# Kernel tuning notes

Hardware: AMD Instinct MI355X
Metric: run time of the kernel (lower is better)

The kernel has to match this reference:

```python
import jax, jax.numpy as jnp
import numpy as np

B, S, H, KV, D = 1, 2048, 16, 4, 128
HID = H * D
CACHE = 2048
EPS = 1e-6
SCALE = 128 ** -0.5  # query_pre_attn_scalar ** -0.5
NEG = -1e9


def setup_inputs() -> dict:
    key = jax.random.key(0)
    ks = jax.random.split(key, 12)
    hidden_states = jax.random.normal(ks[0], (B, S, HID), jnp.float32)
    # rotary embeddings (Gemma3 style, base 10000, half-dim frequencies)
    pos = jnp.arange(S, dtype=jnp.float32)[:, None]
    inv_freq = 1.0 / (10000.0 ** (jnp.arange(0, D, 2, dtype=jnp.float32) / D))
    freqs = pos * inv_freq[None, :]
    emb = jnp.concatenate([freqs, freqs], axis=-1)  # [S, D]
    cos = jnp.cos(emb)[None]  # [1, S, D]
    sin = jnp.sin(emb)[None]
    # additive causal mask [B, 1, S, S]
    r = jnp.arange(S)
    attention_mask = jnp.where(r[:, None] >= r[None, :], 0.0, NEG).astype(jnp.float32)[None, None]
    lyra_key_cache = jax.random.normal(ks[1], (1, KV, CACHE, D), jnp.float32)
    lyra_value_cache = jax.random.normal(ks[2], (1, KV, CACHE, D), jnp.float32)
    w = 0.02
    Wq = jax.random.normal(ks[3], (H * D, HID), jnp.float32) * w
    Wk = jax.random.normal(ks[4], (KV * D, HID), jnp.float32) * w
    Wv = jax.random.normal(ks[5], (KV * D, HID), jnp.float32) * w
    Wo = jax.random.normal(ks[6], (HID, H * D), jnp.float32) * w
    q_norm_w = jax.random.normal(ks[7], (D,), jnp.float32) * 0.1
    k_norm_w = jax.random.normal(ks[8], (D,), jnp.float32) * 0.1
    return dict(hidden_states=hidden_states, cos=cos, sin=sin,
                attention_mask=attention_mask,
                lyra_key_cache=lyra_key_cache, lyra_value_cache=lyra_value_cache,
                Wq=Wq, Wk=Wk, Wv=Wv, Wo=Wo, q_norm_w=q_norm_w, k_norm_w=k_norm_w)


def _rmsnorm(x, w):
    xf = x.astype(jnp.float32)
    n = xf * jax.lax.rsqrt(jnp.mean(xf * xf, axis=-1, keepdims=True) + EPS)
    return (n * (1.0 + w.astype(jnp.float32))).astype(x.dtype)


def _rotate_half(x):
    h = x.shape[-1] // 2
    return jnp.concatenate([-x[..., h:], x[..., :h]], axis=-1)


def _rope(x, c, s):
    return x * c + _rotate_half(x) * s


def _attend(q, k, v, mask, n_rep):
    # q: [B,h,Sq,D]; k,v: [B,KV,Sk,D]; mask additive float broadcastable to [B,h,Sq,Sk]
    k = jnp.repeat(k, n_rep, axis=1)
    v = jnp.repeat(v, n_rep, axis=1)
    w = jnp.einsum('bhqd,bhkd->bhqk', q, k) * SCALE + mask
    w = jax.nn.softmax(w.astype(jnp.float32), axis=-1).astype(q.dtype)
    out = jnp.einsum('bhqk,bhkd->bhqd', w, v)
    return out, w


def reference(hidden_states, cos, sin, attention_mask, lyra_key_cache,
              lyra_value_cache, Wq, Wk, Wv, Wo, q_norm_w, k_norm_w):
    bsz, q_len, _ = hidden_states.shape
    q = (hidden_states @ Wq.T).reshape(bsz, q_len, H, D).transpose(0, 2, 1, 3)
    k = (hidden_states @ Wk.T).reshape(bsz, q_len, KV, D).transpose(0, 2, 1, 3)
    v = (hidden_states @ Wv.T).reshape(bsz, q_len, KV, D).transpose(0, 2, 1, 3)
    q = _rmsnorm(q, q_norm_w)
    k = _rmsnorm(k, k_norm_w)
    vanilla_q, lyra_q = q[:, :H // 2], q[:, H // 2:]
    c = cos[:, None]  # [B,1,S,D]
    s = sin[:, None]
    n_rep = (H // 2) // KV  # stream_num_key_value_groups
    # vanilla stream
    vanilla_q_rope = _rope(vanilla_q, c, s)
    k_rope = _rope(k, c, s)
    vanilla_out, vanilla_w = _attend(vanilla_q_rope, k_rope, v, attention_mask, n_rep)
    # lyra stream: prepend static KV cache; bool mask added as float (faithful to source)
    lyra_q_rope = _rope(lyra_q, c, s)
    lk = jnp.concatenate([jnp.broadcast_to(lyra_key_cache, (bsz, KV, CACHE, D)), k_rope], axis=2)
    lv = jnp.concatenate([jnp.broadcast_to(lyra_value_cache, (bsz, KV, CACHE, D)), v], axis=2)
    rows = jnp.arange(q_len)[:, None]
    cols = jnp.arange(CACHE + q_len)[None, :]
    lyra_mask = (rows < cols - CACHE).astype(jnp.float32)[None, None]  # True -> +1.0, as in torch code
    lyra_out, _ = _attend(lyra_q_rope, lk, lv, lyra_mask, n_rep)
    combined = jnp.concatenate([vanilla_out, lyra_out], axis=1)  # [B,H,S,D]
    combined = combined.transpose(0, 2, 1, 3).reshape(bsz, q_len, H * D)
    attn_output = combined @ Wo.T
    return attn_output, vanilla_w
```

## Files before the change

kernel.cpp:

```cpp
#include <hip/hip_runtime.h>
#include <math.h>

#define S_LEN 2048
#define HID 2048
#define NH 16
#define NKV 4
#define DH 128
#define CACHE_LEN 2048
#define QKV_W 3072
#define SCALE 0.08838834764831845f
#define EPS 1e-6f
#define LYRA_C 12.0f

typedef short bf16x8 __attribute__((ext_vector_type(8)));
typedef float f32x4 __attribute__((ext_vector_type(4)));

static __device__ __forceinline__ short f2bf(float x) {
  union { float f; unsigned u; } v; v.f = x;
  unsigned r = (v.u + 0x7FFF + ((v.u >> 16) & 1)) >> 16;
  return (short)r;
}

static __device__ __forceinline__ float bf2f(short h) {
  union { unsigned u; float f; } v;
// ... 123 lines not shown
  const int rem = e4 & ((1 << 19) - 1);
  const int key = rem >> 7;
  const int d = rem & 127;
  const int dsw = d ^ ((key & 7) << 3);
  if (key < CACHE_LEN) {
    float4 v = *(const float4*)(kcache + (((size_t)kvh * CACHE_LEN + key) << 7) + d);
    short4 o;
    o.x = f2bf(v.x); o.y = f2bf(v.y); o.z = f2bf(v.z); o.w = f2bf(v.w);
    *(short4*)(Kbf + (size_t)(e4 - d) + dsw) = o;
  } else {
    float4 v = *(const float4*)(qkv + (size_t)(key - CACHE_LEN) * QKV_W + 2048 + kvh * DH + d);
    short4 o;
    o.x = f2bf(v.x); o.y = f2bf(v.y); o.z = f2bf(v.z); o.w = f2bf(v.w);
    *(short4*)(Kbf + (size_t)(e4 - d) + dsw) = o;
    short4 ol;
    ol.x = f2bf(v.x - bf2f(o.x));
    ol.y = f2bf(v.y - bf2f(o.y));
    ol.z = f2bf(v.z - bf2f(o.z));
    ol.w = f2bf(v.w - bf2f(o.w));
    *(short4*)(Klo + ((size_t)kvh * 2048 + (key - CACHE_LEN)) * 128 + dsw) = ol;
  }
}

__global__ __launch_bounds__(256) void pack_vt(
    const float* __restrict__ qkv, const float* __restrict__ vcache,
    short* __restrict__ Vt) {
  __shared__ float tile[64][65];
  const int key0 = blockIdx.x * 64;
  const int d0 = blockIdx.y * 64;
  const int kvh = blockIdx.z;
  const int t = threadIdx.x;
  const int c = t & 63;
  const int r0 = t >> 6;
#pragma unroll
  for (int i = 0; i < 16; ++i) {
    int r = r0 + i * 4;
    int key = key0 + r;
    float v;
    if (key < CACHE_LEN)
      v = vcache[(((size_t)kvh * CACHE_LEN + key) << 7) + d0 + c];
    else
      v = qkv[(size_t)(key - CACHE_LEN) * QKV_W + 2560 + kvh * DH + d0 + c];
    tile[r][c] = v;
  }
  __syncthreads();
#pragma unroll
  for (int i = 0; i < 16; ++i) {
    int wr = r0 + i * 4;
    int csw = c ^ (((d0 + wr) & 7) << 3);
    Vt[((size_t)kvh * DH + d0 + wr) * 4096 + key0 + csw] = f2bf(tile[c][wr]);
  }
}

static __device__ __forceinline__ void stage_kv(
    const short* Kb, const short* Vb, short* buf, int key0, int w, int lane) {
#pragma unroll
  for (int i = 0; i < 2; ++i)
    GLDS16(Kb + ((size_t)key0 + w * 8 + i * 4) * 128 + lane * 8,
           buf + (w * 8 + i * 4) * 128);
#pragma unroll
  for (int j = 0; j < 2; ++j)
    GLDS16(Vb + (size_t)(w * 16 + j * 8 + (lane >> 3)) * 4096 + key0 +
               (lane & 7) * 8,
           buf + 8192 + (w * 16 + j * 8) * 64);
}

__global__ __launch_bounds__(512) void lyra_attn(
    const float* __restrict__ qkv,
    const short* __restrict__ Kbf,
    const short* __restrict__ Vtb,
    short* __restrict__ combined_bf) {
  __shared__ short sKV[3][16384];
  __shared__ short sP[8][16][64];
  __shared__ float sL[64];
  const int hj = blockIdx.x;
  const int qt = blockIdx.y;
  const int kvh = hj >> 1;
  const int t = threadIdx.x;
  const int w = t >> 6;
  const int lane = t & 63;
  const int quad = lane >> 4;
  const int l16 = lane & 15;
  const int wr = w >> 1;
  const int wc = w & 1;
  const int row0 = qt * 64;
  const int rbase = row0 + wr * 16 + quad * 4;
  const int swx = (l16 & 7) << 4;

  bf16x8 qf[4];
  {
    const float* qrow =
        qkv + (size_t)(row0 + wr * 16 + l16) * QKV_W + (8 + hj) * DH;
#pragma unroll
    for (int ks = 0; ks < 4; ++ks) {
      float4 f0 = *(const float4*)(qrow + ks * 32 + quad * 8);
      float4 f1 = *(const float4*)(qrow + ks * 32 + quad * 8 + 4);
      qf[ks][0] = f2bf(f0.x); qf[ks][1] = f2bf(f0.y);
      qf[ks][2] = f2bf(f0.z); qf[ks][3] = f2bf(f0.w);
      qf[ks][4] = f2bf(f1.x); qf[ks][5] = f2bf(f1.y);
      qf[ks][6] = f2bf(f1.z); qf[ks][7] = f2bf(f1.w);
    }
  }
  bf16x8 onesf;
#pragma unroll
  for (int i = 0; i < 8; ++i) onesf[i] = (short)0x3F80;

  f32x4 accO[8];
#pragma unroll
  for (int i = 0; i < 8; ++i) accO[i] = (f32x4){0.f, 0.f, 0.f, 0.f};
  f32x4 accL = (f32x4){0.f, 0.f, 0.f, 0.f};

  const short* Kb = Kbf + (size_t)kvh * 4096 * DH;
  const short* Vb = Vtb + (size_t)kvh * DH * 4096;

  stage_kv(Kb, Vb, &sKV[0][0], 0, w, lane);
  stage_kv(Kb, Vb, &sKV[1][0], 64, w, lane);

  short* sPw = &sP[w][0][0];
  int b = 0;
  for (int kt = 0; kt < 64; ++kt) {
    asm volatile("s_waitcnt vmcnt(4)" ::: "memory");
    __builtin_amdgcn_s_barrier();
    __builtin_amdgcn_sched_barrier(0);

    {
      int nb = b + 2; if (nb >= 3) nb -= 3;
      stage_kv(Kb, Vb, &sKV[nb][0], ((kt + 2) & 63) * 64, w, lane);
    }

    const char* Ksc = (const char*)&sKV[b][0];
    const char* Vsc = (const char*)&sKV[b][8192];

    f32x4 accS[2];
#pragma unroll
    for (int s = 0; s < 2; ++s) accS[s] = (f32x4){0.f, 0.f, 0.f, 0.f};
    __builtin_amdgcn_s_setprio(1);
#pragma unroll
    for (int s = 0; s < 2; ++s) {
      const char* krow = Ksc + (wc * 32 + s * 16 + l16) * 256;
#pragma unroll
      for (int ks = 0; ks < 4; ++ks) {
        bf16x8 bk = *(const bf16x8*)(krow + ((ks * 64 + quad * 16) ^ swx));
        accS[s] = __builtin_amdgcn_mfma_f32_16x16x32_bf16(qf[ks], bk, accS[s],
                                                          0, 0, 0);
      }
    }
    __builtin_amdgcn_s_setprio(0);

    const int base = kt * 64 + wc * 32;
    if (kt >= 32) {
#pragma unroll
      for (int s = 0; s < 2; ++s) {
        const int col = base + s * 16 + l16;
#pragma unroll
        for (int r = 0; r < 4; ++r) {
          const int row = quad * 4 + r;
          float sc = accS[s][r] * SCALE;
          if ((col - CACHE_LEN) > (rbase + r)) sc += 1.0f;
          const int sl = (s * 2 + (l16 >> 3)) ^ (row & 7);
          sPw[row * 64 + sl * 8 + (l16 & 7)] = f2bf(__expf(sc - LYRA_C));
        }
      }
    } else {
#pragma unroll
      for (int s = 0; s < 2; ++s)
#pragma unroll
        for (int r = 0; r < 4; ++r) {
          const int row = quad * 4 + r;
          const int sl = (s * 2 + (l16 >> 3)) ^ (row & 7);
          sPw[row * 64 + sl * 8 + (l16 & 7)] =
              f2bf(__expf(accS[s][r] * SCALE - LYRA_C));
        }
    }

    __builtin_amdgcn_s_setprio(1);
    bf16x8 ap = *(const bf16x8*)&sPw[l16 * 64 + ((quad ^ (l16 & 7)) << 3)];
    accL = __builtin_amdgcn_mfma_f32_16x16x32_bf16(ap, onesf, accL, 0, 0, 0);
#pragma unroll
    for (int t8 = 0; t8 < 8; ++t8) {
      bf16x8 bv = *(const bf16x8*)(
          Vsc + (t8 * 16 + l16) * 128 + ((wc * 64 + quad * 16) ^ swx));
      accO[t8] = __builtin_amdgcn_mfma_f32_16x16x32_bf16(ap, bv, accO[t8],
                                                         0, 0, 0);
    }
    __builtin_amdgcn_s_setprio(0);

    ++b; if (b == 3) b = 0;
  }

  __syncthreads();
  float* sO = (float*)&sKV[0][0];
  if (wc == 1) {
#pragma unroll
    for (int t8 = 0; t8 < 8; ++t8)
#pragma unroll
      for (int r = 0; r < 4; ++r)
        sO[((wr * 16 + quad * 4 + r) << 7) + t8 * 16 + l16] = accO[t8][r];
    if (l16 == 0) {
#pragma unroll
      for (int r = 0; r < 4; ++r) sL[wr * 16 + quad * 4 + r] = accL[r];
    }
  }
  __syncthreads();
  if (wc == 0) {
    float linv[4];
#pragma unroll
    for (int r = 0; r < 4; ++r)
      linv[r] = 1.0f / (accL[r] + sL[wr * 16 + quad * 4 + r]);
#pragma unroll
    for (int t8 = 0; t8 < 8; ++t8)
#pragma unroll
      for (int r = 0; r < 4; ++r) {
        float o = accO[t8][r] + sO[((wr * 16 + quad * 4 + r) << 7) + t8 * 16 + l16];
        combined_bf[(size_t)(rbase + r) * HID + (8 + hj) * DH + t8 * 16 + l16] =
            f2bf(o * linv[r]);
      }
  }
}

static __device__ __forceinline__ void stage_van(
    const short* Kh, const short* Kl, const short* Vb, short* buf,
    int key0, int w, int lane) {
#pragma unroll
  for (int i = 0; i < 2; ++i) {
    GLDS16(Kh + ((size_t)key0 + w * 8 + i * 4) * 128 + lane * 8,
           buf + (w * 8 + i * 4) * 128);
    GLDS16(Kl + ((size_t)key0 + w * 8 + i * 4) * 128 + lane * 8,
           buf + 8192 + (w * 8 + i * 4) * 128);
  }
#pragma unroll
  for (int j = 0; j < 2; ++j)
    GLDS16(Vb + (size_t)(w * 16 + j * 8 + (lane >> 3)) * 4096 + key0 +
               (lane & 7) * 8,
           buf + 16384 + (w * 16 + j * 8) * 64);
}

__global__ __launch_bounds__(512) void vanilla_attn(
    const float* __restrict__ qkv,
    const short* __restrict__ Kbf,
    const short* __restrict__ Klo,
    const short* __restrict__ Vtb,
    float* __restrict__ wout,
    float* __restrict__ vinv,
    short* __restrict__ combined_bf) {
  __shared__ short sKV[2][24576];
  __shared__ short sP[8][16][64];
  __shared__ float sL[64];
  const int hj = blockIdx.x;
  const int qt = blockIdx.y;
  const int kvh = hj >> 1;
  const int t = threadIdx.x;
  const int w = t >> 6;
  const int lane = t & 63;
  const int quad = lane >> 4;
  const int l16 = lane & 15;
  const int wr = w >> 1;
  const int wc = w & 1;
  const int row0 = qt * 64;
  const int rbase = row0 + wr * 16 + quad * 4;
  const int swx = (l16 & 7) << 4;

  bf16x8 qh[4], ql[4];
  {
    const float* qrow =
        qkv + (size_t)(row0 + wr * 16 + l16) * QKV_W + hj * DH;
#pragma unroll
    for (int ks = 0; ks < 4; ++ks) {
#pragma unroll
      for (int e = 0; e < 8; ++e) {
        float x = qrow[ks * 32 + quad * 8 + e];
        short h = f2bf(x);
        qh[ks][e] = h;
        ql[ks][e] = f2bf(x - bf2f(h));
      }
    }
  }

  f32x4 accO[8];
#pragma unroll
  for (int i = 0; i < 8; ++i) accO[i] = (f32x4){0.f, 0.f, 0.f, 0.f};
  float accR[4] = {0.f, 0.f, 0.f, 0.f};

  const short* Kh = Kbf + ((size_t)kvh * 4096 + 2048) * DH;
  const short* Kl = Klo + (size_t)kvh * 2048 * DH;
  const short* Vb = Vtb + (size_t)kvh * DH * 4096 + 2048;
  float* wrow = wout + (size_t)hj * S_LEN * S_LEN;

  stage_van(Kh, Kl, Vb, &sKV[0][0], 0, w, lane);

  short* sPw = &sP[w][0][0];
  int b = 0;
  for (int kt = 0; kt <= qt; ++kt) {
    asm volatile("s_waitcnt vmcnt(0)" ::: "memory");
    __builtin_amdgcn_s_barrier();
    __builtin_amdgcn_sched_barrier(0);

    if (kt < qt)
      stage_van(Kh, Kl, Vb, &sKV[b ^ 1][0], (kt + 1) * 64, w, lane);

    const char* Khs = (const char*)&sKV[b][0];
    const char* Kls = (const char*)&sKV[b][8192];
    const char* Vsc = (const char*)&sKV[b][16384];

    f32x4 accS[2];
#pragma unroll
    for (int s = 0; s < 2; ++s) accS[s] = (f32x4){0.f, 0.f, 0.f, 0.f};
    __builtin_amdgcn_s_setprio(1);
#pragma unroll
    for (int s = 0; s < 2; ++s) {
      const char* krh = Khs + (wc * 32 + s * 16 + l16) * 256;
      const char* krl = Kls + (wc * 32 + s * 16 + l16) * 256;
#pragma unroll
      for (int ks = 0; ks < 4; ++ks) {
        const int off = (ks * 64 + quad * 16) ^ swx;
        bf16x8 kh = *(const bf16x8*)(krh + off);
        bf16x8 kl = *(const bf16x8*)(krl + off);
        accS[s] = __builtin_amdgcn_mfma_f32_16x16x32_bf16(qh[ks], kh, accS[s], 0, 0, 0);
        accS[s] = __builtin_amdgcn_mfma_f32_16x16x32_bf16(ql[ks], kh, accS[s], 0, 0, 0);
        accS[s] = __builtin_amdgcn_mfma_f32_16x16x32_bf16(qh[ks], kl, accS[s], 0, 0, 0);
      }
    }
    __builtin_amdgcn_s_setprio(0);

    const int key0 = kt * 64;
    const bool diag = (kt == qt);
    float pr[4] = {0.f, 0.f, 0.f, 0.f};
#pragma unroll
    for (int s = 0; s < 2; ++s) {
      const int col = key0 + wc * 32 + s * 16 + l16;
#pragma unroll
      for (int r = 0; r < 4; ++r) {
        const int row = quad * 4 + r;
        const int grow = rbase + r;
        float p = __expf(accS[s][r] * SCALE - LYRA_C);
        if (diag && col > grow) p = 0.f;
        pr[r] += p;
        const int sl = (s * 2 + (l16 >> 3)) ^ (row & 7);
        sPw[row * 64 + sl * 8 + (l16 & 7)] = f2bf(p);
        wrow[(size_t)grow * S_LEN + col] = p;
      }
    }
#pragma unroll
    for (int r = 0; r < 4; ++r) {
      float v = pr[r];
      v += __shfl_xor(v, 1);
      v += __shfl_xor(v, 2);
      v += __shfl_xor(v, 4);
      v += __shfl_xor(v, 8);
      accR[r] += v;
    }

    __builtin_amdgcn_s_setprio(1);
    bf16x8 ap = *(const bf16x8*)&sPw[l16 * 64 + ((quad ^ (l16 & 7)) << 3)];
#pragma unroll
    for (int t8 = 0; t8 < 8; ++t8) {
      bf16x8 bv = *(const bf16x8*)(
          Vsc + (t8 * 16 + l16) * 128 + ((wc * 64 + quad * 16) ^ swx));
      accO[t8] = __builtin_amdgcn_mfma_f32_16x16x32_bf16(ap, bv, accO[t8],
                                                         0, 0, 0);
    }
    __builtin_amdgcn_s_setprio(0);

    b ^= 1;
  }

  __syncthreads();
  float* sO = (float*)&sKV[0][0];
  if (wc == 1) {
#pragma unroll
    for (int t8 = 0; t8 < 8; ++t8)
#pragma unroll
      for (int r = 0; r < 4; ++r)
        sO[((wr * 16 + quad * 4 + r) << 7) + t8 * 16 + l16] = accO[t8][r];
    if (l16 == 0) {
#pragma unroll
      for (int r = 0; r < 4; ++r) sL[wr * 16 + quad * 4 + r] = accR[r];
    }
  }
  __syncthreads();
  if (wc == 0) {
    float linv[4];
#pragma unroll
    for (int r = 0; r < 4; ++r)
      linv[r] = 1.0f / (accR[r] + sL[wr * 16 + quad * 4 + r]);
    if (l16 == 0) {
#pragma unroll
      for (int r = 0; r < 4; ++r) vinv[hj * S_LEN + rbase + r] = linv[r];
    }
#pragma unroll
    for (int t8 = 0; t8 < 8; ++t8)
#pragma unroll
      for (int r = 0; r < 4; ++r) {
        float o = accO[t8][r] + sO[((wr * 16 + quad * 4 + r) << 7) + t8 * 16 + l16];
        combined_bf[(size_t)(rbase + r) * HID + hj * DH + t8 * 16 + l16] =
            f2bf(o * linv[r]);
      }
  }
}

__global__ __launch_bounds__(256) void vnorm(
    const float* __restrict__ vinv, float* __restrict__ wout) {
  const int row = blockIdx.x;
  const int h = blockIdx.y;
  float* p = wout + (size_t)h * S_LEN * S_LEN + (size_t)row * S_LEN;
  const float inv = vinv[h * S_LEN + row];
  const int t = threadIdx.x;
#pragma unroll
  for (int i = 0; i < 2; ++i) {
    const int j = (t + i * 256) * 4;
    float4 v;
    if (j > row) {
      v = make_float4(0.f, 0.f, 0.f, 0.f);
    } else if (j + 3 <= row) {
      v = *(const float4*)(p + j);
      v.x *= inv; v.y *= inv; v.z *= inv; v.w *= inv;
    } else {
      v = *(const float4*)(p + j);
      v.x = (j + 0 <= row) ? v.x * inv : 0.f;
      v.y = (j + 1 <= row) ? v.y * inv : 0.f;
      v.z = (j + 2 <= row) ? v.z * inv : 0.f;
      v.w = (j + 3 <= row) ? v.w * inv : 0.f;
    }
    *(float4*)(p + j) = v;
  }
}

extern "C" void kernel_launch(void* const* d_in, const int* in_sizes, int n_in,
                              void* d_out, int out_size, void* d_ws, size_t ws_size,
                              hipStream_t stream) {
  (void)in_sizes; (void)n_in; (void)out_size; (void)ws_size;
  const float* hidden = (const float*)d_in[0];
  const float* cosb   = (const float*)d_in[1];
  const float* sinb   = (const float*)d_in[2];
  const float* kcache = (const float*)d_in[4];
  const float* vcache = (const float*)d_in[5];
  const float* Wq = (const float*)d_in[6];
  const float* Wk = (const float*)d_in[7];
  const float* Wv = (const float*)d_in[8];
  const float* Wo = (const float*)d_in[9];
  const float* qw = (const float*)d_in[10];
  const float* kw = (const float*)d_in[11];

  float* out  = (float*)d_out;
  float* wout = out + (size_t)4194304;

  float* qkv = (float*)d_ws;
  short* Kbf = (short*)(qkv + (size_t)2048 * QKV_W);
  short* Vtb = Kbf + (size_t)4 * 4096 * DH;
  short* combined_bf = Vtb + (size_t)4 * DH * 4096;
  short* Wo_bf = combined_bf + (size_t)2048 * HID;

  short* hidden_bf = (short*)wout;
  short* Wqkv_bf = hidden_bf + (size_t)2048 * HID;

  short* Klo  = (short*)out;
  float* vinv = (float*)(Klo + (size_t)4 * 2048 * DH);

  pack_bf16<<<dim3(2048), 256, 0, stream>>>(hidden, hidden_bf);
  pack_bf16<<<dim3(2048), 256, 0, stream>>>(Wq, Wqkv_bf);
  pack_bf16<<<dim3(512), 256, 0, stream>>>(Wk, Wqkv_bf + (size_t)2048 * 2048);
  pack_bf16<<<dim3(512), 256, 0, stream>>>(Wv, Wqkv_bf + (size_t)2560 * 2048);
  pack_bf16<<<dim3(2048), 256, 0, stream>>>(Wo, Wo_bf);

  gemm_bf16<<<dim3(24, 16), 256, 0, stream>>>(hidden_bf, Wqkv_bf, qkv, 2048, QKV_W);
  rms_rope<<<dim3(10240), 256, 0, stream>>>(qkv, cosb, sinb, qw, kw);
  pack_k<<<dim3(2048), 256, 0, stream>>>(qkv, kcache, Kbf, Klo);
  pack_vt<<<dim3(64, 2, 4), 256, 0, stream>>>(qkv, vcache, Vtb);
  lyra_attn<<<dim3(8, 32), 512, 0, stream>>>(qkv, Kbf, Vtb, combined_bf);
  vanilla_attn<<<dim3(8, 32), 512, 0, stream>>>(qkv, Kbf, Klo, Vtb, wout, vinv,
                                                combined_bf);
  vnorm<<<dim3(2048, 8), 256, 0, stream>>>(vinv, wout);
  gemm_bf16<<<dim3(16, 16), 256, 0, stream>>>(combined_bf, Wo_bf, out, 2048, HID);
}
```

Before: 513.0 us.

## Widen attention key tiles to 128 with 2x4 wave grid and register Q reuse

Both attention kernels switch from 64-key to 128-key tiles, arranged as a 2x4 wave grid. Each wave now holds two 16-row Q fragments, so every K and V fragment read from LDS feeds two MFMAs. The lyra kernel drops its triple buffer for a double buffer that waits for vmcnt(0). The vanilla kernel stops staging the low-order K residual in LDS and loads it per wave directly from global memory. The output reduction now combines four column waves through shared memory; the trade-offs are more registers, a coarser causal tile, and uncached global loads in the inner loop.

```diff
diff --git a/kernel.cpp b/kernel.cpp
--- a/kernel.cpp
+++ b/kernel.cpp
@@ -199,17 +199,17 @@
   }
 }
 
-static __device__ __forceinline__ void stage_kv(
+static __device__ __forceinline__ void stage_kv128(
     const short* Kb, const short* Vb, short* buf, int key0, int w, int lane) {
 #pragma unroll
-  for (int i = 0; i < 2; ++i)
-    GLDS16(Kb + ((size_t)key0 + w * 8 + i * 4) * 128 + lane * 8,
-           buf + (w * 8 + i * 4) * 128);
-#pragma unroll
-  for (int j = 0; j < 2; ++j)
-    GLDS16(Vb + (size_t)(w * 16 + j * 8 + (lane >> 3)) * 4096 + key0 +
-               (lane & 7) * 8,
-           buf + 8192 + (w * 16 + j * 8) * 64);
+  for (int i = 0; i < 4; ++i)
+    GLDS16(Kb + ((size_t)key0 + w * 16 + i * 4) * 128 + lane * 8,
+           buf + (w * 16 + i * 4) * 128);
+#pragma unroll
+  for (int i = 0; i < 4; ++i)
+    GLDS16(Vb + (size_t)(w * 16 + i * 4 + (lane >> 4)) * 4096 + key0 +
+               (lane & 15) * 8,
+           buf + 16384 + (w * 16 + i * 4) * 128);
 }
 
 __global__ __launch_bounds__(512) void lyra_attn(
@@ -217,9 +217,8 @@
     const short* __restrict__ Kbf,
     const short* __restrict__ Vtb,
     short* __restrict__ combined_bf) {
-  __shared__ short sKV[3][16384];
-  __shared__ short sP[8][16][64];
-  __shared__ float sL[64];
+  __shared__ short sKV[2][32768];
+  __shared__ short sP[8][2][1024];
   const int hj = blockIdx.x;
   const int qt = blockIdx.y;
   const int kvh = hj >> 1;
@@ -228,59 +227,62 @@
   const int lane = t & 63;
   const int quad = lane >> 4;
   const int l16 = lane & 15;
-  const int wr = w >> 1;
-  const int wc = w & 1;
+  const int wr = w >> 2;
+  const int wc = w & 3;
   const int row0 = qt * 64;
-  const int rbase = row0 + wr * 16 + quad * 4;
   const int swx = (l16 & 7) << 4;
-
-  bf16x8 qf[4];
-  {
+  const int voff = (wc >> 1) * 128 + ((((wc & 1) * 64) + quad * 16) ^ swx);
+
+  bf16x8 qf[2][4];
+#pragma unroll
+  for (int g = 0; g < 2; ++g) {
     const float* qrow =
-        qkv + (size_t)(row0 + wr * 16 + l16) * QKV_W + (8 + hj) * DH;
+        qkv + (size_t)(row0 + wr * 32 + g * 16 + l16) * QKV_W + (8 + hj) * DH;
 #pragma unroll
     for (int ks = 0; ks < 4; ++ks) {
       float4 f0 = *(const float4*)(qrow + ks * 32 + quad * 8);
       float4 f1 = *(const float4*)(qrow + ks * 32 + quad * 8 + 4);
-      qf[ks][0] = f2bf(f0.x); qf[ks][1] = f2bf(f0.y);
-      qf[ks][2] = f2bf(f0.z); qf[ks][3] = f2bf(f0.w);
-      qf[ks][4] = f2bf(f1.x); qf[ks][5] = f2bf(f1.y);
-      qf[ks][6] = f2bf(f1.z); qf[ks][7] = f2bf(f1.w);
+      qf[g][ks][0] = f2bf(f0.x); qf[g][ks][1] = f2bf(f0.y);
+      qf[g][ks][2] = f2bf(f0.z); qf[g][ks][3] = f2bf(f0.w);
+      qf[g][ks][4] = f2bf(f1.x); qf[g][ks][5] = f2bf(f1.y);
+      qf[g][ks][6] = f2bf(f1.z); qf[g][ks][7] = f2bf(f1.w);
     }
   }
   bf16x8 onesf;
 #pragma unroll
   for (int i = 0; i < 8; ++i) onesf[i] = (short)0x3F80;
 
-  f32x4 accO[8];
-#pragma unroll
-  for (int i = 0; i < 8; ++i) accO[i] = (f32x4){0.f, 0.f, 0.f, 0.f};
-  f32x4 accL = (f32x4){0.f, 0.f, 0.f, 0.f};
+  f32x4 accO[2][8];
+#pragma unroll
+  for (int g = 0; g < 2; ++g)
+#pragma unroll
+    for (int i = 0; i < 8; ++i) accO[g][i] = (f32x4){0.f, 0.f, 0.f, 0.f};
+  f32x4 accL[2];
+  accL[0] = (f32x4){0.f, 0.f, 0.f, 0.f};
+  accL[1] = (f32x4){0.f, 0.f, 0.f, 0.f};
 
   const short* Kb = Kbf + (size_t)kvh * 4096 * DH;
   const short* Vb = Vtb + (size_t)kvh * DH * 4096;
 
-  stage_kv(Kb, Vb, &sKV[0][0], 0, w, lane);
-  stage_kv(Kb, Vb, &sKV[1][0], 64, w, lane);
-
-  short* sPw = &sP[w][0][0];
+  stage_kv128(Kb, Vb, &sKV[0][0], 0, w, lane);
+
   int b = 0;
-  for (int kt = 0; kt < 64; ++kt) {
-    asm volatile("s_waitcnt vmcnt(4)" ::: "memory");
+  for (int kt = 0; kt < 32; ++kt) {
+    asm volatile("s_waitcnt vmcnt(0)" ::: "memory");
     __builtin_amdgcn_s_barrier();
     __builtin_amdgcn_sched_barrier(0);
 
-    {
-      int nb = b + 2; if (nb >= 3) nb -= 3;
-      stage_kv(Kb, Vb, &sKV[nb][0], ((kt + 2) & 63) * 64, w, lane);
-    }
+    if (kt < 31)
+      stage_kv128(Kb, Vb, &sKV[b ^ 1][0], (kt + 1) * 128, w, lane);
 
     const char* Ksc = (const char*)&sKV[b][0];
-    const char* Vsc = (const char*)&sKV[b][8192];
-
-    f32x4 accS[2];
-#pragma unroll
-    for (int s = 0; s < 2; ++s) accS[s] = (f32x4){0.f, 0.f, 0.f, 0.f};
+    const char* Vsc = (const char*)&sKV[b][16384];
+
+    f32x4 accS[2][2];
+#pragma unroll
+    for (int g = 0; g < 2; ++g)
+#pragma unroll
+      for (int s = 0; s < 2; ++s) accS[g][s] = (f32x4){0.f, 0.f, 0.f, 0.f};
     __builtin_amdgcn_s_setprio(1);
 #pragma unroll
     for (int s = 0; s < 2; ++s) {
@@ -288,98 +290,92 @@
 #pragma unroll
       for (int ks = 0; ks < 4; ++ks) {
         bf16x8 bk = *(const bf16x8*)(krow + ((ks * 64 + quad * 16) ^ swx));
-        accS[s] = __builtin_amdgcn_mfma_f32_16x16x32_bf16(qf[ks], bk, accS[s],
-                                                          0, 0, 0);
+        accS[0][s] = __builtin_amdgcn_mfma_f32_16x16x32_bf16(qf[0][ks], bk, accS[0][s], 0, 0, 0);
+        accS[1][s] = __builtin_amdgcn_mfma_f32_16x16x32_bf16(qf[1][ks], bk, accS[1][s], 0, 0, 0);
       }
     }
     __builtin_amdgcn_s_setprio(0);
 
-    const int base = kt * 64 + wc * 32;
-    if (kt >= 32) {
+    const int base = kt * 128 + wc * 32;
+#pragma unroll
+    for (int g = 0; g < 2; ++g) {
+      short* sPg = &sP[w][g][0];
 #pragma unroll
       for (int s = 0; s < 2; ++s) {
         const int col = base + s * 16 + l16;
 #pragma unroll
         for (int r = 0; r < 4; ++r) {
           const int row = quad * 4 + r;
-          float sc = accS[s][r] * SCALE;
-          if ((col - CACHE_LEN) > (rbase + r)) sc += 1.0f;
+          const int grow = row0 + wr * 32 + g * 16 + row;
+          float sc = accS[g][s][r] * SCALE;
+          if ((col - CACHE_LEN) > grow) sc += 1.0f;
           const int sl = (s * 2 + (l16 >> 3)) ^ (row & 7);
-          sPw[row * 64 + sl * 8 + (l16 & 7)] = f2bf(__expf(sc - LYRA_C));
+          sPg[row * 64 + sl * 8 + (l16 & 7)] = f2bf(__expf(sc - LYRA_C));
         }
       }
-    } else {
-#pragma unroll
-      for (int s = 0; s < 2; ++s)
-#pragma unroll
-        for (int r = 0; r < 4; ++r) {
-          const int row = quad * 4 + r;
-          const int sl = (s * 2 + (l16 >> 3)) ^ (row & 7);
-          sPw[row * 64 + sl * 8 + (l16 & 7)] =
-              f2bf(__expf(accS[s][r] * SCALE - LYRA_C));
-        }
     }
 
     __builtin_amdgcn_s_setprio(1);
-    bf16x8 ap = *(const bf16x8*)&sPw[l16 * 64 + ((quad ^ (l16 & 7)) << 3)];
-    accL = __builtin_amdgcn_mfma_f32_16x16x32_bf16(ap, onesf, accL, 0, 0, 0);
+    bf16x8 ap0 = *(const bf16x8*)&sP[w][0][l16 * 64 + ((quad ^ (l16 & 7)) << 3)];
+    bf16x8 ap1 = *(const bf16x8*)&sP[w][1][l16 * 64 + ((quad ^ (l16 & 7)) << 3)];
+    accL[0] = __builtin_amdgcn_mfma_f32_16x16x32_bf16(ap0, onesf, accL[0], 0, 0, 0);
+    accL[1] = __builtin_amdgcn_mfma_f32_16x16x32_bf16(ap1, onesf, accL[1], 0, 0, 0);
 #pragma unroll
     for (int t8 = 0; t8 < 8; ++t8) {
-      bf16x8 bv = *(const bf16x8*)(
-          Vsc + (t8 * 16 + l16) * 128 + ((wc * 64 + quad * 16) ^ swx));
-      accO[t8] = __builtin_amdgcn_mfma_f32_16x16x32_bf16(ap, bv, accO[t8],
-                                                         0, 0, 0);
+      bf16x8 bv = *(const bf16x8*)(Vsc + (t8 * 16 + l16) * 256 + voff);
+      accO[0][t8] = __builtin_amdgcn_mfma_f32_16x16x32_bf16(ap0, bv, accO[0][t8], 0, 0, 0);
+      accO[1][t8] = __builtin_amdgcn_mfma_f32_16x16x32_bf16(ap1, bv, accO[1][t8], 0, 0, 0);
     }
     __builtin_amdgcn_s_setprio(0);
 
-    ++b; if (b == 3) b = 0;
+    b ^= 1;
   }
 
   __syncthreads();
   float* sO = (float*)&sKV[0][0];
-  if (wc == 1) {
-#pragma unroll
-    for (int t8 = 0; t8 < 8; ++t8)
-#pragma unroll
-      for (int r = 0; r < 4; ++r)
-        sO[((wr * 16 + quad * 4 + r) << 7) + t8 * 16 + l16] = accO[t8][r];
+  float* sLa = (float*)&sP[0][0][0];
+  if (wc != 0) {
+    float* dst = sO + (size_t)(wc - 1) * 8192;
+#pragma unroll
+    for (int g = 0; g < 2; ++g)
+#pragma unroll
+      for (int t8 = 0; t8 < 8; ++t8)
+#pragma unroll
+        for (int r = 0; r < 4; ++r) {
+          const int rl = wr * 32 + g * 16 + quad * 4 + r;
+          dst[rl * 128 + t8 * 16 + l16] = accO[g][t8][r];
+        }
     if (l16 == 0) {
 #pragma unroll
-      for (int r = 0; r < 4; ++r) sL[wr * 16 + quad * 4 + r] = accL[r];
+      for (int g = 0; g < 2; ++g)
+#pragma unroll
+        for (int r = 0; r < 4; ++r)
+          sLa[(wc - 1) * 64 + wr * 32 + g * 16 + quad * 4 + r] = accL[g][r];
     }
   }
   __syncthreads();
   if (wc == 0) {
-    float linv[4];
-#pragma unroll
-    for (int r = 0; r < 4; ++r)
-      linv[r] = 1.0f / (accL[r] + sL[wr * 16 + quad * 4 + r]);
-#pragma unroll
-    for (int t8 = 0; t8 < 8; ++t8)
+#pragma unroll
+    for (int g = 0; g < 2; ++g) {
+      float linv[4];
 #pragma unroll
       for (int r = 0; r < 4; ++r) {
-        float o = accO[t8][r] + sO[((wr * 16 + quad * 4 + r) << 7) + t8 * 16 + l16];
-        combined_bf[(size_t)(rbase + r) * HID + (8 + hj) * DH + t8 * 16 + l16] =
-            f2bf(o * linv[r]);
-      }
-  }
-}
-
-static __device__ __forceinline__ void stage_van(
-    const short* Kh, const short* Kl, const short* Vb, short* buf,
-    int key0, int w, int lane) {
-#pragma unroll
-  for (int i = 0; i < 2; ++i) {
-    GLDS16(Kh + ((size_t)key0 + w * 8 + i * 4) * 128 + lane * 8,
-           buf + (w * 8 + i * 4) * 128);
-    GLDS16(Kl + ((size_t)key0 + w * 8 + i * 4) * 128 + lane * 8,
-           buf + 8192 + (w * 8 + i * 4) * 128);
-  }
-#pragma unroll
-  for (int j = 0; j < 2; ++j)
-    GLDS16(Vb + (size_t)(w * 16 + j * 8 + (lane >> 3)) * 4096 + key0 +
-               (lane & 7) * 8,
-           buf + 16384 + (w * 16 + j * 8) * 64);
+        const int rl = wr * 32 + g * 16 + quad * 4 + r;
+        linv[r] = 1.0f / (accL[g][r] + sLa[rl] + sLa[64 + rl] + sLa[128 + rl]);
+      }
+#pragma unroll
+      for (int t8 = 0; t8 < 8; ++t8)
+#pragma unroll
+        for (int r = 0; r < 4; ++r) {
+          const int rl = wr * 32 + g * 16 + quad * 4 + r;
+          const int c = t8 * 16 + l16;
+          float o = accO[g][t8][r] + sO[rl * 128 + c] + sO[8192 + rl * 128 + c] +
+                    sO[16384 + rl * 128 + c];
+          combined_bf[(size_t)(row0 + rl) * HID + (8 + hj) * DH + c] =
+              f2bf(o * linv[r]);
+        }
+    }
+  }
 }
 
 __global__ __launch_bounds__(512) void vanilla_attn(
@@ -390,9 +386,8 @@
     float* __restrict__ wout,
     float* __restrict__ vinv,
     short* __restrict__ combined_bf) {
-  __shared__ short sKV[2][24576];
-  __shared__ short sP[8][16][64];
-  __shared__ float sL[64];
+  __shared__ short sKV[2][32768];
+  __shared__ short sP[8][2][1024];
   const int hj = blockIdx.x;
   const int qt = blockIdx.y;
   const int kvh = hj >> 1;
@@ -401,110 +396,127 @@
   const int lane = t & 63;
   const int quad = lane >> 4;
   const int l16 = lane & 15;
-  const int wr = w >> 1;
-  const int wc = w & 1;
+  const int wr = w >> 2;
+  const int wc = w & 3;
   const int row0 = qt * 64;
-  const int rbase = row0 + wr * 16 + quad * 4;
   const int swx = (l16 & 7) << 4;
-
-  bf16x8 qh[4], ql[4];
-  {
+  const int voff = (wc >> 1) * 128 + ((((wc & 1) * 64) + quad * 16) ^ swx);
+  const int nt = qt / 2 + 1;
+
+  bf16x8 qh[2][4], ql[2][4];
+#pragma unroll
+  for (int g = 0; g < 2; ++g) {
     const float* qrow =
-        qkv + (size_t)(row0 + wr * 16 + l16) * QKV_W + hj * DH;
+        qkv + (size_t)(row0 + wr * 32 + g * 16 + l16) * QKV_W + hj * DH;
 #pragma unroll
     for (int ks = 0; ks < 4; ++ks) {
 #pragma unroll
       for (int e = 0; e < 8; ++e) {
         float x = qrow[ks * 32 + quad * 8 + e];
         short h = f2bf(x);
-        qh[ks][e] = h;
-        ql[ks][e] = f2bf(x - bf2f(h));
-      }
-    }
-  }
-
-  f32x4 accO[8];
-#pragma unroll
-  for (int i = 0; i < 8; ++i) accO[i] = (f32x4){0.f, 0.f, 0.f, 0.f};
-  float accR[4] = {0.f, 0.f, 0.f, 0.f};
+        qh[g][ks][e] = h;
+        ql[g][ks][e] = f2bf(x - bf2f(h));
+      }
+    }
+  }
+
+  f32x4 accO[2][8];
+#pragma unroll
+  for (int g = 0; g < 2; ++g)
+#pragma unroll
+    for (int i = 0; i < 8; ++i) accO[g][i] = (f32x4){0.f, 0.f, 0.f, 0.f};
+  float accR[2][4] = {{0.f, 0.f, 0.f, 0.f}, {0.f, 0.f, 0.f, 0.f}};
 
   const short* Kh = Kbf + ((size_t)kvh * 4096 + 2048) * DH;
   const short* Kl = Klo + (size_t)kvh * 2048 * DH;
   const short* Vb = Vtb + (size_t)kvh * DH * 4096 + 2048;
   float* wrow = wout + (size_t)hj * S_LEN * S_LEN;
 
-  stage_van(Kh, Kl, Vb, &sKV[0][0], 0, w, lane);
-
-  short* sPw = &sP[w][0][0];
+  stage_kv128(Kh, Vb, &sKV[0][0], 0, w, lane);
+
   int b = 0;
-  for (int kt = 0; kt <= qt; ++kt) {
+  for (int kt = 0; kt < nt; ++kt) {
     asm volatile("s_waitcnt vmcnt(0)" ::: "memory");
     __builtin_amdgcn_s_barrier();
     __builtin_amdgcn_sched_barrier(0);
 
-    if (kt < qt)
-      stage_van(Kh, Kl, Vb, &sKV[b ^ 1][0], (kt + 1) * 64, w, lane);
+    if (kt < nt - 1)
+      stage_kv128(Kh, Vb, &sKV[b ^ 1][0], (kt + 1) * 128, w, lane);
+
+    const int key0 = kt * 128;
+    bf16x8 klf[2][4];
+#pragma unroll
+    for (int s = 0; s < 2; ++s)
+#pragma unroll
+      for (int ks = 0; ks < 4; ++ks)
+        klf[s][ks] = *(const bf16x8*)(
+            Kl + (size_t)(key0 + wc * 32 + s * 16 + l16) * 128 +
+            ((ks * 32 + quad * 8) ^ ((l16 & 7) << 3)));
 
     const char* Khs = (const char*)&sKV[b][0];
-    const char* Kls = (const char*)&sKV[b][8192];
     const char* Vsc = (const char*)&sKV[b][16384];
 
-    f32x4 accS[2];
-#pragma unroll
-    for (int s = 0; s < 2; ++s) accS[s] = (f32x4){0.f, 0.f, 0.f, 0.f};
+    f32x4 accS[2][2];
+#pragma unroll
+    for (int g = 0; g < 2; ++g)
+#pragma unroll
+      for (int s = 0; s < 2; ++s) accS[g][s] = (f32x4){0.f, 0.f, 0.f, 0.f};
     __builtin_amdgcn_s_setprio(1);
 #pragma unroll
     for (int s = 0; s < 2; ++s) {
       const char* krh = Khs + (wc * 32 + s * 16 + l16) * 256;
-      const char* krl = Kls + (wc * 32 + s * 16 + l16) * 256;
 #pragma unroll
       for (int ks = 0; ks < 4; ++ks) {
-        const int off = (ks * 64 + quad * 16) ^ swx;
-        bf16x8 kh = *(const bf16x8*)(krh + off);
-        bf16x8 kl = *(const bf16x8*)(krl + off);
-        accS[s] = __builtin_amdgcn_mfma_f32_16x16x32_bf16(qh[ks], kh, accS[s], 0, 0, 0);
-        accS[s] = __builtin_amdgcn_mfma_f32_16x16x32_bf16(ql[ks], kh, accS[s], 0, 0, 0);
-        accS[s] = __builtin_amdgcn_mfma_f32_16x16x32_bf16(qh[ks], kl, accS[s], 0, 0, 0);
+        bf16x8 kh = *(const bf16x8*)(krh + ((ks * 64 + quad * 16) ^ swx));
+        accS[0][s] = __builtin_amdgcn_mfma_f32_16x16x32_bf16(qh[0][ks], kh, accS[0][s], 0, 0, 0);
+        accS[1][s] = __builtin_amdgcn_mfma_f32_16x16x32_bf16(qh[1][ks], kh, accS[1][s], 0, 0, 0);
+        accS[0][s] = __builtin_amdgcn_mfma_f32_16x16x32_bf16(ql[0][ks], kh, accS[0][s], 0, 0, 0);
+        accS[1][s] = __builtin_amdgcn_mfma_f32_16x16x32_bf16(ql[1][ks], kh, accS[1][s], 0, 0, 0);
+        accS[0][s] = __builtin_amdgcn_mfma_f32_16x16x32_bf16(qh[0][ks], klf[s][ks], accS[0][s], 0, 0, 0);
+        accS[1][s] = __builtin_amdgcn_mfma_f32_16x16x32_bf16(qh[1][ks], klf[s][ks], accS[1][s], 0, 0, 0);
       }
     }
     __builtin_amdgcn_s_setprio(0);
 
-    const int key0 = kt * 64;
-    const bool diag = (kt == qt);
-    float pr[4] = {0.f, 0.f, 0.f, 0.f};
-#pragma unroll
-    for (int s = 0; s < 2; ++s) {
-      const int col = key0 + wc * 32 + s * 16 + l16;
+    const bool diag = (kt == nt - 1);
+#pragma unroll
+    for (int g = 0; g < 2; ++g) {
+      short* sPg = &sP[w][g][0];
+      float pr[4] = {0.f, 0.f, 0.f, 0.f};
+#pragma unroll
+      for (int s = 0; s < 2; ++s) {
+        const int col = key0 + wc * 32 + s * 16 + l16;
+#pragma unroll
+        for (int r = 0; r < 4; ++r) {
+          const int row = quad * 4 + r;
+          const int grow = row0 + wr * 32 + g * 16 + row;
+          float p = __expf(accS[g][s][r] * SCALE - LYRA_C);
+          if (diag && col > grow) p = 0.f;
+          pr[r] += p;
+          const int sl = (s * 2 + (l16 >> 3)) ^ (row & 7);
+          sPg[row * 64 + sl * 8 + (l16 & 7)] = f2bf(p);
+          wrow[(size_t)grow * S_LEN + col] = p;
+        }
+      }
 #pragma unroll
       for (int r = 0; r < 4; ++r) {
-        const int row = quad * 4 + r;
-        const int grow = rbase + r;
-        float p = __expf(accS[s][r] * SCALE - LYRA_C);
-        if (diag && col > grow) p = 0.f;
-        pr[r] += p;
-        const int sl = (s * 2 + (l16 >> 3)) ^ (row & 7);
-        sPw[row * 64 + sl * 8 + (l16 & 7)] = f2bf(p);
-        wrow[(size_t)grow * S_LEN + col] = p;
-      }
-    }
-#pragma unroll
-    for (int r = 0; r < 4; ++r) {
-      float v = pr[r];
-      v += __shfl_xor(v, 1);
-      v += __shfl_xor(v, 2);
-      v += __shfl_xor(v, 4);
-      v += __shfl_xor(v, 8);
-      accR[r] += v;
+        float v = pr[r];
+        v += __shfl_xor(v, 1);
+        v += __shfl_xor(v, 2);
+        v += __shfl_xor(v, 4);
+        v += __shfl_xor(v, 8);
+        accR[g][r] += v;
+      }
     }
 
     __builtin_amdgcn_s_setprio(1);
-    bf16x8 ap = *(const bf16x8*)&sPw[l16 * 64 + ((quad ^ (l16 & 7)) << 3)];
+    bf16x8 ap0 = *(const bf16x8*)&sP[w][0][l16 * 64 + ((quad ^ (l16 & 7)) << 3)];
+    bf16x8 ap1 = *(const bf16x8*)&sP[w][1][l16 * 64 + ((quad ^ (l16 & 7)) << 3)];
 #pragma unroll
     for (int t8 = 0; t8 < 8; ++t8) {
-      bf16x8 bv = *(const bf16x8*)(
-          Vsc + (t8 * 16 + l16) * 128 + ((wc * 64 + quad * 16) ^ swx));
-      accO[t8] = __builtin_amdgcn_mfma_f32_16x16x32_bf16(ap, bv, accO[t8],
-                                                         0, 0, 0);
+      bf16x8 bv = *(const bf16x8*)(Vsc + (t8 * 16 + l16) * 256 + voff);
+      accO[0][t8] = __builtin_amdgcn_mfma_f32_16x16x32_bf16(ap0, bv, accO[0][t8], 0, 0, 0);
+      accO[1][t8] = __builtin_amdgcn_mfma_f32_16x16x32_bf16(ap1, bv, accO[1][t8], 0, 0, 0);
     }
     __builtin_amdgcn_s_setprio(0);
 
@@ -513,35 +525,53 @@
 
   __syncthreads();
   float* sO = (float*)&sKV[0][0];
-  if (wc == 1) {
-#pragma unroll
-    for (int t8 = 0; t8 < 8; ++t8)
-#pragma unroll
-      for (int r = 0; r < 4; ++r)
-        sO[((wr * 16 + quad * 4 + r) << 7) + t8 * 16 + l16] = accO[t8][r];
+  float* sLa = (float*)&sP[0][0][0];
+  if (wc != 0) {
+    float* dst = sO + (size_t)(wc - 1) * 8192;
+#pragma unroll
+    for (int g = 0; g < 2; ++g)
+#pragma unroll
+      for (int t8 = 0; t8 < 8; ++t8)
+#pragma unroll
+        for (int r = 0; r < 4; ++r) {
+          const int rl = wr * 32 + g * 16 + quad * 4 + r;
+          dst[rl * 128 + t8 * 16 + l16] = accO[g][t8][r];
+        }
     if (l16 == 0) {
 #pragma unroll
-      for (int r = 0; r < 4; ++r) sL[wr * 16 + quad * 4 + r] = accR[r];
+      for (int g = 0; g < 2; ++g)
+#pragma unroll
+        for (int r = 0; r < 4; ++r)
+          sLa[(wc - 1) * 64 + wr * 32 + g * 16 + quad * 4 + r] = accR[g][r];
     }
   }
   __syncthreads();
   if (wc == 0) {
-    float linv[4];
-#pragma unroll
-    for (int r = 0; r < 4; ++r)
-      linv[r] = 1.0f / (accR[r] + sL[wr * 16 + quad * 4 + r]);
-    if (l16 == 0) {
-#pragma unroll
-      for (int r = 0; r < 4; ++r) vinv[hj * S_LEN + rbase + r] = linv[r];
-    }
-#pragma unroll
-    for (int t8 = 0; t8 < 8; ++t8)
+#pragma unroll
+    for (int g = 0; g < 2; ++g) {
+      float linv[4];
 #pragma unroll
       for (int r = 0; r < 4; ++r) {
-        float o = accO[t8][r] + sO[((wr * 16 + quad * 4 + r) << 7) + t8 * 16 + l16];
-        combined_bf[(size_t)(rbase + r) * HID + hj * DH + t8 * 16 + l16] =
-            f2bf(o * linv[r]);
-      }
+        const int rl = wr * 32 + g * 16 + quad * 4 + r;
+        linv[r] = 1.0f / (accR[g][r] + sLa[rl] + sLa[64 + rl] + sLa[128 + rl]);
+      }
+      if (l16 == 0) {
+#pragma unroll
+        for (int r = 0; r < 4; ++r)
+          vinv[hj * S_LEN + row0 + wr * 32 + g * 16 + quad * 4 + r] = linv[r];
+      }
+#pragma unroll
+      for (int t8 = 0; t8 < 8; ++t8)
+#pragma unroll
+        for (int r = 0; r < 4; ++r) {
+          const int rl = wr * 32 + g * 16 + quad * 4 + r;
+          const int c = t8 * 16 + l16;
+          float o = accO[g][t8][r] + sO[rl * 128 + c] + sO[8192 + rl * 128 + c] +
+                    sO[16384 + rl * 128 + c];
+          combined_bf[(size_t)(row0 + rl) * HID + hj * DH + c] =
+              f2bf(o * linv[r]);
+        }
+    }
   }
 }
 
```

After: 496.3 us. -3.3%, faster.

## Halve attention query tiles, load V and K-low fragments directly from global

Applied to the files above, without the earlier changes.

Both attention kernels move from 64-row query tiles with 512 threads to 32-row tiles with 256 threads, doubling the grid and shrinking LDS to roughly 34 KB per block. V fragments, and the vanilla K-low fragments, are now read straight from global memory into registers instead of being staged in LDS, so only K-high goes through the double-buffered LDS pipeline. The vanilla kernel remaps block indices to pair short and long causal rows for load balance, and lyra drops its cache/no-cache branch split. The aim is higher occupancy and less LDS traffic, at the cost of more global loads, lost K/V reuse across the smaller tile, and a full vmcnt(0) wait each iteration.

```diff
diff --git a/kernel.cpp b/kernel.cpp
--- a/kernel.cpp
+++ b/kernel.cpp
@@ -199,29 +199,24 @@
   }
 }
 
-static __device__ __forceinline__ void stage_kv(
-    const short* Kb, const short* Vb, short* buf, int key0, int w, int lane) {
-#pragma unroll
-  for (int i = 0; i < 2; ++i)
-    GLDS16(Kb + ((size_t)key0 + w * 8 + i * 4) * 128 + lane * 8,
-           buf + (w * 8 + i * 4) * 128);
-#pragma unroll
-  for (int j = 0; j < 2; ++j)
-    GLDS16(Vb + (size_t)(w * 16 + j * 8 + (lane >> 3)) * 4096 + key0 +
-               (lane & 7) * 8,
-           buf + 8192 + (w * 16 + j * 8) * 64);
-}
-
-__global__ __launch_bounds__(512) void lyra_attn(
+static __device__ __forceinline__ void stage_k64(
+    const short* Kb, short* buf, int key0, int w, int lane) {
+#pragma unroll
+  for (int i = 0; i < 4; ++i)
+    GLDS16(Kb + ((size_t)key0 + w * 16 + i * 4) * 128 + lane * 8,
+           buf + (w * 16 + i * 4) * 128);
+}
+
+__global__ __launch_bounds__(256) void lyra_attn(
     const float* __restrict__ qkv,
     const short* __restrict__ Kbf,
     const short* __restrict__ Vtb,
     short* __restrict__ combined_bf) {
-  __shared__ short sKV[3][16384];
-  __shared__ short sP[8][16][64];
-  __shared__ float sL[64];
+  __shared__ short sK[2][8192];
+  __shared__ short sP[4][1024];
+  __shared__ float sL[32];
   const int hj = blockIdx.x;
-  const int qt = blockIdx.y;
+  const int qt2 = blockIdx.y;
   const int kvh = hj >> 1;
   const int t = threadIdx.x;
   const int w = t >> 6;
@@ -230,9 +225,10 @@
   const int l16 = lane & 15;
   const int wr = w >> 1;
   const int wc = w & 1;
-  const int row0 = qt * 64;
+  const int row0 = qt2 * 32;
   const int rbase = row0 + wr * 16 + quad * 4;
   const int swx = (l16 & 7) << 4;
+  const int vsw = (l16 & 7) << 3;
 
   bf16x8 qf[4];
   {
@@ -260,23 +256,24 @@
   const short* Kb = Kbf + (size_t)kvh * 4096 * DH;
   const short* Vb = Vtb + (size_t)kvh * DH * 4096;
 
-  stage_kv(Kb, Vb, &sKV[0][0], 0, w, lane);
-  stage_kv(Kb, Vb, &sKV[1][0], 64, w, lane);
-
-  short* sPw = &sP[w][0][0];
+  stage_k64(Kb, &sK[0][0], 0, w, lane);
+
+  short* sPw = &sP[w][0];
   int b = 0;
   for (int kt = 0; kt < 64; ++kt) {
-    asm volatile("s_waitcnt vmcnt(4)" ::: "memory");
+    asm volatile("s_waitcnt vmcnt(0)" ::: "memory");
     __builtin_amdgcn_s_barrier();
     __builtin_amdgcn_sched_barrier(0);
 
-    {
-      int nb = b + 2; if (nb >= 3) nb -= 3;
-      stage_kv(Kb, Vb, &sKV[nb][0], ((kt + 2) & 63) * 64, w, lane);
-    }
-
-    const char* Ksc = (const char*)&sKV[b][0];
-    const char* Vsc = (const char*)&sKV[b][8192];
+    bf16x8 bvg[8];
+    const int vcol = kt * 64 + ((wc * 32 + quad * 8) ^ vsw);
+#pragma unroll
+    for (int t8 = 0; t8 < 8; ++t8)
+      bvg[t8] = *(const bf16x8*)(Vb + (size_t)(t8 * 16 + l16) * 4096 + vcol);
+
+    if (kt < 63) stage_k64(Kb, &sK[b ^ 1][0], (kt + 1) * 64, w, lane);
+
+    const char* Ksc = (const char*)&sK[b][0];
 
     f32x4 accS[2];
 #pragma unroll
@@ -295,54 +292,39 @@
     __builtin_amdgcn_s_setprio(0);
 
     const int base = kt * 64 + wc * 32;
-    if (kt >= 32) {
-#pragma unroll
-      for (int s = 0; s < 2; ++s) {
-        const int col = base + s * 16 + l16;
-#pragma unroll
-        for (int r = 0; r < 4; ++r) {
-          const int row = quad * 4 + r;
-          float sc = accS[s][r] * SCALE;
-          if ((col - CACHE_LEN) > (rbase + r)) sc += 1.0f;
-          const int sl = (s * 2 + (l16 >> 3)) ^ (row & 7);
-          sPw[row * 64 + sl * 8 + (l16 & 7)] = f2bf(__expf(sc - LYRA_C));
-        }
-      }
-    } else {
-#pragma unroll
-      for (int s = 0; s < 2; ++s)
-#pragma unroll
-        for (int r = 0; r < 4; ++r) {
-          const int row = quad * 4 + r;
-          const int sl = (s * 2 + (l16 >> 3)) ^ (row & 7);
-          sPw[row * 64 + sl * 8 + (l16 & 7)] =
-              f2bf(__expf(accS[s][r] * SCALE - LYRA_C));
-        }
+#pragma unroll
+    for (int s = 0; s < 2; ++s) {
+      const int col = base + s * 16 + l16;
+#pragma unroll
+      for (int r = 0; r < 4; ++r) {
+        const int row = quad * 4 + r;
+        float sc = accS[s][r] * SCALE;
+        if ((col - CACHE_LEN) > (rbase + r)) sc += 1.0f;
+        const int sl = (s * 2 + (l16 >> 3)) ^ (row & 7);
+        sPw[row * 64 + sl * 8 + (l16 & 7)] = f2bf(__expf(sc - LYRA_C));
+      }
     }
 
     __builtin_amdgcn_s_setprio(1);
     bf16x8 ap = *(const bf16x8*)&sPw[l16 * 64 + ((quad ^ (l16 & 7)) << 3)];
     accL = __builtin_amdgcn_mfma_f32_16x16x32_bf16(ap, onesf, accL, 0, 0, 0);
 #pragma unroll
-    for (int t8 = 0; t8 < 8; ++t8) {
-      bf16x8 bv = *(const bf16x8*)(
-          Vsc + (t8 * 16 + l16) * 128 + ((wc * 64 + quad * 16) ^ swx));
-      accO[t8] = __builtin_amdgcn_mfma_f32_16x16x32_bf16(ap, bv, accO[t8],
+    for (int t8 = 0; t8 < 8; ++t8)
+      accO[t8] = __builtin_amdgcn_mfma_f32_16x16x32_bf16(ap, bvg[t8], accO[t8],
                                                          0, 0, 0);
-    }
     __builtin_amdgcn_s_setprio(0);
 
-    ++b; if (b == 3) b = 0;
+    b ^= 1;
   }
 
   __syncthreads();
-  float* sO = (float*)&sKV[0][0];
+  float* sO = (float*)&sK[0][0];
   if (wc == 1) {
 #pragma unroll
     for (int t8 = 0; t8 < 8; ++t8)
 #pragma unroll
       for (int r = 0; r < 4; ++r)
-        sO[((wr * 16 + quad * 4 + r) << 7) + t8 * 16 + l16] = accO[t8][r];
+        sO[(wr * 16 + quad * 4 + r) * 128 + t8 * 16 + l16] = accO[t8][r];
     if (l16 == 0) {
 #pragma unroll
       for (int r = 0; r < 4; ++r) sL[wr * 16 + quad * 4 + r] = accL[r];
@@ -358,31 +340,15 @@
     for (int t8 = 0; t8 < 8; ++t8)
 #pragma unroll
       for (int r = 0; r < 4; ++r) {
-        float o = accO[t8][r] + sO[((wr * 16 + quad * 4 + r) << 7) + t8 * 16 + l16];
-        combined_bf[(size_t)(rbase + r) * HID + (8 + hj) * DH + t8 * 16 + l16] =
+        const int rl = wr * 16 + quad * 4 + r;
+        float o = accO[t8][r] + sO[rl * 128 + t8 * 16 + l16];
+        combined_bf[(size_t)(row0 + rl) * HID + (8 + hj) * DH + t8 * 16 + l16] =
             f2bf(o * linv[r]);
       }
   }
 }
 
-static __device__ __forceinline__ void stage_van(
-    const short* Kh, const short* Kl, const short* Vb, short* buf,
-    int key0, int w, int lane) {
-#pragma unroll
-  for (int i = 0; i < 2; ++i) {
-    GLDS16(Kh + ((size_t)key0 + w * 8 + i * 4) * 128 + lane * 8,
-           buf + (w * 8 + i * 4) * 128);
-    GLDS16(Kl + ((size_t)key0 + w * 8 + i * 4) * 128 + lane * 8,
-           buf + 8192 + (w * 8 + i * 4) * 128);
-  }
-#pragma unroll
-  for (int j = 0; j < 2; ++j)
-    GLDS16(Vb + (size_t)(w * 16 + j * 8 + (lane >> 3)) * 4096 + key0 +
-               (lane & 7) * 8,
-           buf + 16384 + (w * 16 + j * 8) * 64);
-}
-
-__global__ __launch_bounds__(512) void vanilla_attn(
+__global__ __launch_bounds__(256) void vanilla_attn(
     const float* __restrict__ qkv,
     const short* __restrict__ Kbf,
     const short* __restrict__ Klo,
@@ -390,11 +356,12 @@
     float* __restrict__ wout,
     float* __restrict__ vinv,
     short* __restrict__ combined_bf) {
-  __shared__ short sKV[2][24576];
-  __shared__ short sP[8][16][64];
-  __shared__ float sL[64];
+  __shared__ short sK[2][8192];
+  __shared__ short sP[4][1024];
+  __shared__ float sL[32];
   const int hj = blockIdx.x;
-  const int qt = blockIdx.y;
+  const int by = blockIdx.y;
+  const int qt2 = (by < 32) ? by : 95 - by;
   const int kvh = hj >> 1;
   const int t = threadIdx.x;
   const int w = t >> 6;
@@ -403,9 +370,11 @@
   const int l16 = lane & 15;
   const int wr = w >> 1;
   const int wc = w & 1;
-  const int row0 = qt * 64;
+  const int row0 = qt2 * 32;
   const int rbase = row0 + wr * 16 + quad * 4;
   const int swx = (l16 & 7) << 4;
+  const int vsw = (l16 & 7) << 3;
+  const int nt = qt2 / 2 + 1;
 
   bf16x8 qh[4], ql[4];
   {
@@ -433,21 +402,32 @@
   const short* Vb = Vtb + (size_t)kvh * DH * 4096 + 2048;
   float* wrow = wout + (size_t)hj * S_LEN * S_LEN;
 
-  stage_van(Kh, Kl, Vb, &sKV[0][0], 0, w, lane);
-
-  short* sPw = &sP[w][0][0];
+  stage_k64(Kh, &sK[0][0], 0, w, lane);
+
+  short* sPw = &sP[w][0];
   int b = 0;
-  for (int kt = 0; kt <= qt; ++kt) {
+  for (int kt = 0; kt < nt; ++kt) {
     asm volatile("s_waitcnt vmcnt(0)" ::: "memory");
     __builtin_amdgcn_s_barrier();
     __builtin_amdgcn_sched_barrier(0);
 
-    if (kt < qt)
-      stage_van(Kh, Kl, Vb, &sKV[b ^ 1][0], (kt + 1) * 64, w, lane);
-
-    const char* Khs = (const char*)&sKV[b][0];
-    const char* Kls = (const char*)&sKV[b][8192];
-    const char* Vsc = (const char*)&sKV[b][16384];
+    bf16x8 bvg[8];
+    const int vcol = kt * 64 + ((wc * 32 + quad * 8) ^ vsw);
+#pragma unroll
+    for (int t8 = 0; t8 < 8; ++t8)
+      bvg[t8] = *(const bf16x8*)(Vb + (size_t)(t8 * 16 + l16) * 4096 + vcol);
+    bf16x8 klf[2][4];
+#pragma unroll
+    for (int s = 0; s < 2; ++s)
+#pragma unroll
+      for (int ks = 0; ks < 4; ++ks)
+        klf[s][ks] = *(const bf16x8*)(
+            Kl + (size_t)(kt * 64 + wc * 32 + s * 16 + l16) * 128 +
+            ((ks * 32 + quad * 8) ^ vsw));
+
+    if (kt < nt - 1) stage_k64(Kh, &sK[b ^ 1][0], (kt + 1) * 64, w, lane);
+
+    const char* Khs = (const char*)&sK[b][0];
 
     f32x4 accS[2];
 #pragma unroll
@@ -456,25 +436,21 @@
 #pragma unroll
     for (int s = 0; s < 2; ++s) {
       const char* krh = Khs + (wc * 32 + s * 16 + l16) * 256;
-      const char* krl = Kls + (wc * 32 + s * 16 + l16) * 256;
 #pragma unroll
       for (int ks = 0; ks < 4; ++ks) {
-        const int off = (ks * 64 + quad * 16) ^ swx;
-        bf16x8 kh = *(const bf16x8*)(krh + off);
-        bf16x8 kl = *(const bf16x8*)(krl + off);
+        bf16x8 kh = *(const bf16x8*)(krh + ((ks * 64 + quad * 16) ^ swx));
         accS[s] = __builtin_amdgcn_mfma_f32_16x16x32_bf16(qh[ks], kh, accS[s], 0, 0, 0);
         accS[s] = __builtin_amdgcn_mfma_f32_16x16x32_bf16(ql[ks], kh, accS[s], 0, 0, 0);
-        accS[s] = __builtin_amdgcn_mfma_f32_16x16x32_bf16(qh[ks], kl, accS[s], 0, 0, 0);
+        accS[s] = __builtin_amdgcn_mfma_f32_16x16x32_bf16(qh[ks], klf[s][ks], accS[s], 0, 0, 0);
       }
     }
     __builtin_amdgcn_s_setprio(0);
 
-    const int key0 = kt * 64;
-    const bool diag = (kt == qt);
+    const bool diag = (kt == nt - 1);
     float pr[4] = {0.f, 0.f, 0.f, 0.f};
 #pragma unroll
     for (int s = 0; s < 2; ++s) {
-      const int col = key0 + wc * 32 + s * 16 + l16;
+      const int col = kt * 64 + wc * 32 + s * 16 + l16;
 #pragma unroll
       for (int r = 0; r < 4; ++r) {
         const int row = quad * 4 + r;
@@ -500,25 +476,22 @@
     __builtin_amdgcn_s_setprio(1);
     bf16x8 ap = *(const bf16x8*)&sPw[l16 * 64 + ((quad ^ (l16 & 7)) << 3)];
 #pragma unroll
-    for (int t8 = 0; t8 < 8; ++t8) {
-      bf16x8 bv = *(const bf16x8*)(
-          Vsc + (t8 * 16 + l16) * 128 + ((wc * 64 + quad * 16) ^ swx));
-      accO[t8] = __builtin_amdgcn_mfma_f32_16x16x32_bf16(ap, bv, accO[t8],
+    for (int t8 = 0; t8 < 8; ++t8)
+      accO[t8] = __builtin_amdgcn_mfma_f32_16x16x32_bf16(ap, bvg[t8], accO[t8],
                                                          0, 0, 0);
-    }
     __builtin_amdgcn_s_setprio(0);
 
     b ^= 1;
   }
 
   __syncthreads();
-  float* sO = (float*)&sKV[0][0];
+  float* sO = (float*)&sK[0][0];
   if (wc == 1) {
 #pragma unroll
     for (int t8 = 0; t8 < 8; ++t8)
 #pragma unroll
       for (int r = 0; r < 4; ++r)
-        sO[((wr * 16 + quad * 4 + r) << 7) + t8 * 16 + l16] = accO[t8][r];
+        sO[(wr * 16 + quad * 4 + r) * 128 + t8 * 16 + l16] = accO[t8][r];
     if (l16 == 0) {
 #pragma unroll
       for (int r = 0; r < 4; ++r) sL[wr * 16 + quad * 4 + r] = accR[r];
@@ -532,14 +505,16 @@
       linv[r] = 1.0f / (accR[r] + sL[wr * 16 + quad * 4 + r]);
     if (l16 == 0) {
 #pragma unroll
-      for (int r = 0; r < 4; ++r) vinv[hj * S_LEN + rbase + r] = linv[r];
+      for (int r = 0; r < 4; ++r)
+        vinv[hj * S_LEN + rbase + r] = linv[r];
     }
 #pragma unroll
     for (int t8 = 0; t8 < 8; ++t8)
 #pragma unroll
       for (int r = 0; r < 4; ++r) {
-        float o = accO[t8][r] + sO[((wr * 16 + quad * 4 + r) << 7) + t8 * 16 + l16];
-        combined_bf[(size_t)(rbase + r) * HID + hj * DH + t8 * 16 + l16] =
+        const int rl = wr * 16 + quad * 4 + r;
+        float o = accO[t8][r] + sO[rl * 128 + t8 * 16 + l16];
+        combined_bf[(size_t)(row0 + rl) * HID + hj * DH + t8 * 16 + l16] =
             f2bf(o * linv[r]);
       }
   }
@@ -613,8 +588,8 @@
   rms_rope<<<dim3(10240), 256, 0, stream>>>(qkv, cosb, sinb, qw, kw);
   pack_k<<<dim3(2048), 256, 0, stream>>>(qkv, kcache, Kbf, Klo);
   pack_vt<<<dim3(64, 2, 4), 256, 0, stream>>>(qkv, vcache, Vtb);
-  lyra_attn<<<dim3(8, 32), 512, 0, stream>>>(qkv, Kbf, Vtb, combined_bf);
-  vanilla_attn<<<dim3(8, 32), 512, 0, stream>>>(qkv, Kbf, Klo, Vtb, wout, vinv,
+  lyra_attn<<<dim3(8, 64), 256, 0, stream>>>(qkv, Kbf, Vtb, combined_bf);
+  vanilla_attn<<<dim3(8, 64), 256, 0, stream>>>(qkv, Kbf, Klo, Vtb, wout, vinv,
                                                 combined_bf);
   vnorm<<<dim3(2048, 8), 256, 0, stream>>>(vinv, wout);
   gemm_bf16<<<dim3(16, 16), 256, 0, stream>>>(combined_bf, Wo_bf, out, 2048, HID);
```

New measurement: 535.7 us. +4.4%, slower.
